# Performance work log

Hardware: AMD Instinct MI355X
Metric: run time of the kernel (lower is better)

## Reference

```python
import jax, jax.numpy as jnp
import numpy as np
from jax import lax

# Resolved Optuna hyperparameters
NPOINTS = (512, 256, 128)
RADII = (0.2, 0.4, 0.8)
KS = (32, 32, 32)
BN_EPS = 1e-5


def _fps_single(pts, npoint):
    """Farthest point sampling on one cloud. pts: (N,3) -> (npoint,) int32."""
    N = pts.shape[0]
    def step(carry, _):
        dists, last = carry
        d = jnp.sum((pts - pts[last]) ** 2, axis=-1)
        dists = jnp.minimum(dists, d)
        nxt = jnp.argmax(dists).astype(jnp.int32)
        return (dists, nxt), last
    init = (jnp.full((N,), 1e10, pts.dtype), jnp.int32(0))
    (_, _), idx = lax.scan(step, init, None, length=npoint)
    return idx


def _set_abstraction(xyz, feat, W, b, radius, k, npoint):
    """xyz: (B,N,3), feat: (B,N,C_in) -> new_xyz (B,S,3), new_feat (B,S,C_out)."""
    B, N, _ = xyz.shape
    fps_idx = jax.vmap(lambda p: _fps_single(p, npoint))(xyz)          # (B,S)
    new_xyz = jax.vmap(lambda x, i: x[i])(xyz, fps_idx)                # (B,S,3)
    # ball query: squared distances centers -> all points
    d2 = jnp.sum((new_xyz[:, :, None, :] - xyz[:, None, :, :]) ** 2, axis=-1)  # (B,S,N)
    valid = d2 <= radius * radius
    ar = jnp.arange(N, dtype=jnp.int32)
    gi = jnp.where(valid, ar[None, None, :], N)                        # invalid -> N
    gi = jnp.sort(gi, axis=-1)[:, :, :k]                               # first k in index order
    first = gi[:, :, :1]
    gi = jnp.where(gi == N, first, gi)                                 # pad with first valid (center itself)
    g_xyz = jax.vmap(lambda x, i: x[i])(xyz, gi)                       # (B,S,k,3)
    rel = g_xyz - new_xyz[:, :, None, :]
    g_feat = jax.vmap(lambda x, i: x[i])(feat, gi)                     # (B,S,k,C_in)
    h = jnp.concatenate([rel, g_feat], axis=-1)                        # (B,S,k,3+C_in)
    h = jax.nn.relu(jnp.einsum('bskc,co->bsko', h, W) + b)
    return new_xyz, jnp.max(h, axis=2)                                 # max-pool over group


def _bn(x, g, b):
    # nn.BatchNorm1d training-mode forward (batch statistics, biased var)
    m = x.mean(axis=0)
    v = x.var(axis=0)
    return (x - m) * lax.rsqrt(v + BN_EPS) * g + b


def setup_inputs() -> dict:
    key = jax.random.key(0)
    ks = jax.random.split(key, 8)
    def w(k, i, o):
        return (jax.random.normal(k, (i, o), jnp.float32) / np.sqrt(i)).astype(jnp.float32)
    return dict(
        points=jax.random.uniform(ks[0], (16, 4096, 3), jnp.float32),
        W1=w(ks[1], 3 + 3, 64),   b1=jnp.zeros((64,), jnp.float32),
        W2=w(ks[2], 64 + 3, 128), b2=jnp.zeros((128,), jnp.float32),
        W3=w(ks[3], 128 + 3, 256), b3=jnp.zeros((256,), jnp.float32),
        fc1_w=w(ks[4], 256, 256), fc1_b=jnp.zeros((256,), jnp.float32),
        fc2_w=w(ks[5], 256, 128), fc2_b=jnp.zeros((128,), jnp.float32),
        fc3_w=w(ks[6], 128, 12),  fc3_b=jnp.zeros((12,), jnp.float32),
        bn1_g=jnp.ones((256,), jnp.float32), bn1_b=jnp.zeros((256,), jnp.float32),
        bn2_g=jnp.ones((128,), jnp.float32), bn2_b=jnp.zeros((128,), jnp.float32),
    )


def reference(points, W1, b1, W2, b2, W3, b3, fc1_w, fc1_b, fc2_w, fc2_b,
              fc3_w, fc3_b, bn1_g, bn1_b, bn2_g, bn2_b):
    B = points.shape[0]
    xyz, feat = points, points
    for (W, bb, r, k, s) in ((W1, b1, RADII[0], KS[0], NPOINTS[0]),
                             (W2, b2, RADII[1], KS[1], NPOINTS[1]),
                             (W3, b3, RADII[2], KS[2], NPOINTS[2])):
        xyz, feat = _set_abstraction(xyz, feat, W, bb, r, k, s)
    f = jnp.max(feat, axis=1)                                          # (B, ch3)
    x = jax.nn.relu(_bn(f @ fc1_w + fc1_b, bn1_g, bn1_b))              # dropout: eval-mode identity
    x = jax.nn.relu(_bn(x @ fc2_w + fc2_b, bn2_g, bn2_b))
    x = x @ fc3_w + fc3_b
    return x.reshape(B, 4, 3)
```

## Files before the change

kernel.cpp:

```cpp
#include <hip/hip_runtime.h>
#include <hip/hip_bf16.h>


#define B_SZ 16

template<int CTRL>
__device__ __forceinline__ float dpp_mv(float v) {
    const int i = __float_as_int(v);
    const int r = __builtin_amdgcn_update_dpp(i, i, CTRL, 0xf, 0xf, false);
    return __int_as_float(r);
}

template<int N, int NPOINT, int BLOCK>
__global__ __launch_bounds__(BLOCK) void fps_kernel(
    const float* __restrict__ xyz,
    float* __restrict__ newxyz)
{
    constexpr int P  = N / BLOCK;
    constexpr int NW = BLOCK / 64;
    __shared__ float4 part[2][NW];

    const int b = blockIdx.x, tid = threadIdx.x;
    const int lane = tid & 63, w = tid >> 6;
    const float* xb = xyz + (size_t)b * N * 3;

    float px[P], py[P], pz[P], dd[P];
    const int base = tid * P;
#pragma unroll
    for (int i = 0; i < P; i++) {
        px[i] = xb[(base + i) * 3 + 0];
        py[i] = xb[(base + i) * 3 + 1];
        pz[i] = xb[(base + i) * 3 + 2];
        dd[i] = 1e10f;
    }
    float lx = xb[0], ly = xb[1], lz = xb[2];
    if (tid == 0) {
        float* o = newxyz + (size_t)b * NPOINT * 3;
        o[0] = lx; o[1] = ly; o[2] = lz;
    }

    for (int s = 1; s < NPOINT; s++) {
        float bv = -1.0f, bx = 0.0f, by = 0.0f, bz = 0.0f;
#pragma unroll
        for (int i = 0; i < P; i++) {
            const float dx = px[i] - lx, dy = py[i] - ly, dz = pz[i] - lz;
            const float d2 = __fadd_rn(__fadd_rn(__fmul_rn(dx, dx), __fmul_rn(dy, dy)),
                                       __fmul_rn(dz, dz));
            const float nd = fminf(dd[i], d2);
            dd[i] = nd;
            const bool gt = nd > bv;
            bv = gt ? nd : bv;
            bx = gt ? px[i] : bx;
            by = gt ? py[i] : by;
            bz = gt ? pz[i] : bz;
        }
        float v = bv;
        v = fmaxf(v, dpp_mv<0x111>(v));
        v = fmaxf(v, dpp_mv<0x112>(v));
        v = fmaxf(v, dpp_mv<0x114>(v));
        v = fmaxf(v, dpp_mv<0x118>(v));
        v = fmaxf(v, dpp_mv<0x142>(v));
        v = fmaxf(v, dpp_mv<0x143>(v));
        const float wmax = __uint_as_float(__builtin_amdgcn_readlane(__float_as_uint(v), 63));
        const unsigned long long mset = __ballot(bv == wmax);
        const int li = __ffsll(mset) - 1;
        const int buf = s & 1;
        if (lane == li) part[buf][w] = make_float4(bv, bx, by, bz);
        __syncthreads();
        float cv = -1.0f;
#pragma unroll
        for (int q = 0; q < NW; q++) {
            const float4 pq = part[buf][q];
            const bool gt = pq.x > cv;
            cv = gt ? pq.x : cv;
            lx = gt ? pq.y : lx;
            ly = gt ? pq.z : ly;
            lz = gt ? pq.w : lz;
        }
        if (tid == 0) {
            float* o = newxyz + ((size_t)b * NPOINT + s) * 3;
            o[0] = lx; o[1] = ly; o[2] = lz;
        }
    }
}

template<int N, int S, int CF, int COUT, int R>
__global__ __launch_bounds__(64) void sa_kernel(
    const float* __restrict__ xyz,
    const float* __restrict__ feat,
    const float* __restrict__ cent,
    const float* __restrict__ W,
    const float* __restrict__ bias,
    float* __restrict__ outf,
    const float r2)
{
    constexpr int K    = 32;
    constexpr int JT   = 16;
    constexpr int CIN  = CF + 3;
    constexpr int CINP = (CIN + 3) & ~3;
    constexpr int C4   = CIN & ~3;
    __shared__ int   gi[K];
    __shared__ float h[JT * CINP];

    const int s = blockIdx.x, b = blockIdx.y;
    const int lane = threadIdx.x;

    const float* xb = xyz  + (size_t)b * N * 3;
    const float* fb = feat + (size_t)b * N * CF;
    const float cx = cent[((size_t)b * S + s) * 3 + 0];
    const float cy = cent[((size_t)b * S + s) * 3 + 1];
    const float cz = cent[((size_t)b * S + s) * 3 + 2];

    constexpr int RND = N / 256;
    int total = 0, g0 = 0;
    for (int r0 = 0; r0 < RND; r0++) {
        if (total >= K) break;
        float xs[4], ys[4], zs[4];
#pragma unroll
        for (int c4 = 0; c4 < 4; c4++) {
            const int p = (r0 * 4 + c4) * 64 + lane;
            xs[c4] = xb[p * 3 + 0];
            ys[c4] = xb[p * 3 + 1];
            zs[c4] = xb[p * 3 + 2];
        }
#pragma unroll
        for (int c4 = 0; c4 < 4; c4++) {
            const int p = (r0 * 4 + c4) * 64 + lane;
            const float dx = xs[c4] - cx, dy = ys[c4] - cy, dz = zs[c4] - cz;
            const float d2 = __fadd_rn(__fadd_rn(__fmul_rn(dx, dx), __fmul_rn(dy, dy)),
                                       __fmul_rn(dz, dz));
            const bool v = (d2 <= r2);
            const unsigned long long bal = __ballot(v);
            if (total == 0 && bal != 0ull) g0 = (r0 * 4 + c4) * 64 + (__ffsll(bal) - 1);
            const int pos = total + __popcll(bal & ((1ull << lane) - 1ull));
            if (v && pos < K) gi[pos] = p;
            total += __popcll(bal);
        }
    }
    if (lane == 0 && total < K) {
        for (int q = total; q < K; q++) gi[q] = g0;
    }
    __syncthreads();

    float m[R];
#pragma unroll
    for (int r = 0; r < R; r++) m[r] = -1e30f;

    for (int pass = 0; pass < K / JT; pass++) {
        for (int jj = 0; jj < JT; jj++) {
            const int idx = gi[pass * JT + jj];
            for (int c = lane; c < CIN; c += 64) {
                float val;
                if (c < 3) {
                    const float cc = (c == 0) ? cx : ((c == 1) ? cy : cz);
                    val = xb[idx * 3 + c] - cc;
                } else {
                    val = fb[(size_t)idx * CF + (c - 3)];
                }
                h[jj * CINP + c] = val;
            }
        }
        __syncthreads();

        float acc[JT][R];
#pragma unroll
        for (int jj = 0; jj < JT; jj++)
#pragma unroll
            for (int r = 0; r < R; r++) acc[jj][r] = 0.0f;

        const float* wp = W + lane;
        int c = 0;
        for (; c < C4; c += 4) {
            float wv[4][R];
#pragma unroll
            for (int q = 0; q < 4; q++)
#pragma unroll
                for (int r = 0; r < R; r++)
                    wv[q][r] = wp[(size_t)(c + q) * COUT + r * 64];
#pragma unroll
            for (int jj = 0; jj < JT; jj++) {
                const float4 hv = *(const float4*)&h[jj * CINP + c];
#pragma unroll
                for (int r = 0; r < R; r++) {
                    acc[jj][r] = fmaf(hv.x, wv[0][r], acc[jj][r]);
                    acc[jj][r] = fmaf(hv.y, wv[1][r], acc[jj][r]);
                    acc[jj][r] = fmaf(hv.z, wv[2][r], acc[jj][r]);
                    acc[jj][r] = fmaf(hv.w, wv[3][r], acc[jj][r]);
                }
            }
        }
        for (; c < CIN; c++) {
            float wv[R];
#pragma unroll
            for (int r = 0; r < R; r++) wv[r] = wp[(size_t)c * COUT + r * 64];
#pragma unroll
            for (int jj = 0; jj < JT; jj++) {
                const float hv = h[jj * CINP + c];
#pragma unroll
                for (int r = 0; r < R; r++)
                    acc[jj][r] = fmaf(hv, wv[r], acc[jj][r]);
            }
        }
#pragma unroll
        for (int jj = 0; jj < JT; jj++)
#pragma unroll
            for (int r = 0; r < R; r++) m[r] = fmaxf(m[r], acc[jj][r]);
        __syncthreads();
    }

#pragma unroll
    for (int r = 0; r < R; r++) {
        const int o = r * 64 + lane;
        outf[((size_t)b * S + s) * COUT + o] = fmaxf(bias[o] + m[r], 0.0f);
    }
}

__global__ __launch_bounds__(256) void maxpool_kernel(
    const float* __restrict__ feat,
    float* __restrict__ out)
{
    const int b = blockIdx.x, o = threadIdx.x;
    const float* fb = feat + (size_t)b * 128 * 256 + o;
    float m = fb[0];
#pragma unroll 4
    for (int s1 = 1; s1 < 128; s1++) m = fmaxf(m, fb[(size_t)s1 * 256]);
    out[b * 256 + o] = m;
}

__global__ __launch_bounds__(256) void head_kernel(
    const float* __restrict__ f,
    const float* __restrict__ fc1_w, const float* __restrict__ fc1_b,
    const float* __restrict__ fc2_w, const float* __restrict__ fc2_b,
    const float* __restrict__ fc3_w, const float* __restrict__ fc3_b,
    const float* __restrict__ bn1_g, const float* __restrict__ bn1_b,
    const float* __restrict__ bn2_g, const float* __restrict__ bn2_b,
    float* __restrict__ out)
{
    __shared__ float fl[16 * 257];
    __shared__ float x1[16 * 257];
    __shared__ float x2[16 * 129];
    const int tid = threadIdx.x;

    for (int idx = tid; idx < 16 * 256; idx += 256) {
        const int r = idx >> 8, c = idx & 255;
        fl[r * 257 + c] = f[idx];
    }
    __syncthreads();

    {
        const int r = tid >> 4, g = tid & 15;
        float acc[16];
#pragma unroll
        for (int i = 0; i < 16; i++) acc[i] = fc1_b[g * 16 + i];
        const float* wrow = fc1_w + g * 16;
        for (int c = 0; c < 256; c++) {
            const float fv = fl[r * 257 + c];
            const float4* w4 = (const float4*)(wrow + (size_t)c * 256);
#pragma unroll
            for (int q = 0; q < 4; q++) {
                const float4 wv = w4[q];
                acc[q * 4 + 0] = fmaf(fv, wv.x, acc[q * 4 + 0]);
                acc[q * 4 + 1] = fmaf(fv, wv.y, acc[q * 4 + 1]);
                acc[q * 4 + 2] = fmaf(fv, wv.z, acc[q * 4 + 2]);
                acc[q * 4 + 3] = fmaf(fv, wv.w, acc[q * 4 + 3]);
            }
        }
#pragma unroll
        for (int i = 0; i < 16; i++) x1[r * 257 + g * 16 + i] = acc[i];
    }
    __syncthreads();
    {
        const int o = tid;
        float v[16];
#pragma unroll
        for (int r = 0; r < 16; r++) v[r] = x1[r * 257 + o];
        float m = 0.0f;
#pragma unroll
        for (int r = 0; r < 16; r++) m += v[r];
        m *= (1.0f / 16.0f);
        float var = 0.0f;
#pragma unroll
        for (int r = 0; r < 16; r++) { const float d = v[r] - m; var += d * d; }
        var *= (1.0f / 16.0f);
        const float sc = bn1_g[o] / sqrtf(var + 1e-5f);
        const float sh = bn1_b[o];
#pragma unroll
        for (int r = 0; r < 16; r++)
            x1[r * 257 + o] = fmaxf((v[r] - m) * sc + sh, 0.0f);
    }
    __syncthreads();
    {
        const int r = tid >> 4, g = tid & 15;
        float acc[8];
#pragma unroll
        for (int i = 0; i < 8; i++) acc[i] = fc2_b[g * 8 + i];
        const float* wrow = fc2_w + g * 8;
        for (int c = 0; c < 256; c++) {
            const float fv = x1[r * 257 + c];
            const float4* w4 = (const float4*)(wrow + (size_t)c * 128);
#pragma unroll
            for (int q = 0; q < 2; q++) {
                const float4 wv = w4[q];
                acc[q * 4 + 0] = fmaf(fv, wv.x, acc[q * 4 + 0]);
                acc[q * 4 + 1] = fmaf(fv, wv.y, acc[q * 4 + 1]);
                acc[q * 4 + 2] = fmaf(fv, wv.z, acc[q * 4 + 2]);
                acc[q * 4 + 3] = fmaf(fv, wv.w, acc[q * 4 + 3]);
            }
        }
#pragma unroll
        for (int i = 0; i < 8; i++) x2[r * 129 + g * 8 + i] = acc[i];
    }
    __syncthreads();
    if (tid < 128) {
        const int o = tid;
        float v[16];
#pragma unroll
        for (int r = 0; r < 16; r++) v[r] = x2[r * 129 + o];
        float m = 0.0f;
#pragma unroll
        for (int r = 0; r < 16; r++) m += v[r];
        m *= (1.0f / 16.0f);
        float var = 0.0f;
#pragma unroll
        for (int r = 0; r < 16; r++) { const float d = v[r] - m; var += d * d; }
        var *= (1.0f / 16.0f);
        const float sc = bn2_g[o] / sqrtf(var + 1e-5f);
        const float sh = bn2_b[o];
#pragma unroll
        for (int r = 0; r < 16; r++)
            x2[r * 129 + o] = fmaxf((v[r] - m) * sc + sh, 0.0f);
    }
    __syncthreads();
    if (tid < 192) {
        const int r = tid / 12, j = tid - r * 12;
        float acc = fc3_b[j];
        for (int c = 0; c < 128; c++)
            acc = fmaf(x2[r * 129 + c], fc3_w[c * 12 + j], acc);
        out[r * 12 + j] = acc;
    }
}

extern "C" void kernel_launch(void* const* d_in, const int* in_sizes, int n_in,
                              void* d_out, int out_size, void* d_ws, size_t ws_size,
                              hipStream_t stream) {
    const float* points = (const float*)d_in[0];
    const float* W1     = (const float*)d_in[1];
    const float* b1     = (const float*)d_in[2];
    const float* W2     = (const float*)d_in[3];
    const float* b2     = (const float*)d_in[4];
    const float* W3     = (const float*)d_in[5];
    const float* b3     = (const float*)d_in[6];
    const float* fc1_w  = (const float*)d_in[7];
    const float* fc1_b  = (const float*)d_in[8];
    const float* fc2_w  = (const float*)d_in[9];
    const float* fc2_b  = (const float*)d_in[10];
    const float* fc3_w  = (const float*)d_in[11];
    const float* fc3_b  = (const float*)d_in[12];
    const float* bn1_g  = (const float*)d_in[13];
    const float* bn1_b  = (const float*)d_in[14];
    const float* bn2_g  = (const float*)d_in[15];
    const float* bn2_b  = (const float*)d_in[16];
    float* out = (float*)d_out;

    float* ws   = (float*)d_ws;
    float* nx1  = ws;
    float* f1   = nx1 + 24576;
    float* nx2  = f1  + 524288;
    float* f2   = nx2 + 12288;
    float* nx3  = f2  + 524288;
    float* f3   = nx3 + 6144;
    float* fmx  = f3  + 524288;

    fps_kernel<4096, 512, 512><<<B_SZ, 512, 0, stream>>>(points, nx1);
    sa_kernel<4096, 512, 3, 64, 1><<<dim3(512, B_SZ), 64, 0, stream>>>(
        points, points, nx1, W1, b1, f1, (float)(0.2 * 0.2));
    fps_kernel<512, 256, 512><<<B_SZ, 512, 0, stream>>>(nx1, nx2);
    sa_kernel<512, 256, 64, 128, 2><<<dim3(256, B_SZ), 64, 0, stream>>>(
        nx1, f1, nx2, W2, b2, f2, (float)(0.4 * 0.4));
    fps_kernel<256, 128, 256><<<B_SZ, 256, 0, stream>>>(nx2, nx3);
    sa_kernel<256, 128, 128, 256, 4><<<dim3(128, B_SZ), 64, 0, stream>>>(
        nx2, f2, nx3, W3, b3, f3, (float)(0.8 * 0.8));
    maxpool_kernel<<<B_SZ, 256, 0, stream>>>(f3, fmx);
    head_kernel<<<1, 256, 0, stream>>>(fmx, fc1_w, fc1_b, fc2_w, fc2_b,
                                       fc3_w, fc3_b, bn1_g, bn1_b, bn2_g, bn2_b,
                                       out);
}
```

Before: 876.1 us.

## Use single-wave FPS for small clouds and tree-reduce per-thread argmax

The per-point argmax tracking in farthest point sampling becomes a tree max over the per-thread distance array, and the winning coordinates are recovered from a shared-memory copy of the cloud. Stages 2 and 3 (512 and 256 points) move to a new single-wave kernel that needs no __syncthreads, broadcasting the winner with readlane. Stage 1 drops from 512 to 256 threads, so each thread handles more points. The aim is to cut the per-step block synchronisation and serial select chain that dominate this latency-bound loop, at the cost of fewer threads doing more work each.

```diff
diff --git a/kernel.cpp b/kernel.cpp
--- a/kernel.cpp
+++ b/kernel.cpp
@@ -11,61 +11,82 @@
     return __int_as_float(r);
 }
 
+__device__ __forceinline__ float wave_max_f32(float x) {
+    float v = x;
+    v = fmaxf(v, dpp_mv<0x111>(v));
+    v = fmaxf(v, dpp_mv<0x112>(v));
+    v = fmaxf(v, dpp_mv<0x114>(v));
+    v = fmaxf(v, dpp_mv<0x118>(v));
+    v = fmaxf(v, dpp_mv<0x142>(v));
+    v = fmaxf(v, dpp_mv<0x143>(v));
+    return __uint_as_float(__builtin_amdgcn_readlane(__float_as_uint(v), 63));
+}
+
+__device__ __forceinline__ float read_lane_f32(float v, int l) {
+    return __uint_as_float(__builtin_amdgcn_readlane(__float_as_uint(v), l));
+}
+
 template<int N, int NPOINT, int BLOCK>
-__global__ __launch_bounds__(BLOCK) void fps_kernel(
+__global__ __launch_bounds__(BLOCK, 1) void fps_kernel(
     const float* __restrict__ xyz,
     float* __restrict__ newxyz)
 {
     constexpr int P  = N / BLOCK;
     constexpr int NW = BLOCK / 64;
+    __shared__ float pts[N * 3];
     __shared__ float4 part[2][NW];
 
     const int b = blockIdx.x, tid = threadIdx.x;
     const int lane = tid & 63, w = tid >> 6;
     const float* xb = xyz + (size_t)b * N * 3;
 
+    for (int t = tid; t < N * 3; t += BLOCK) pts[t] = xb[t];
+    __syncthreads();
+
     float px[P], py[P], pz[P], dd[P];
     const int base = tid * P;
 #pragma unroll
     for (int i = 0; i < P; i++) {
-        px[i] = xb[(base + i) * 3 + 0];
-        py[i] = xb[(base + i) * 3 + 1];
-        pz[i] = xb[(base + i) * 3 + 2];
+        px[i] = pts[(base + i) * 3 + 0];
+        py[i] = pts[(base + i) * 3 + 1];
+        pz[i] = pts[(base + i) * 3 + 2];
         dd[i] = 1e10f;
     }
-    float lx = xb[0], ly = xb[1], lz = xb[2];
+    float lx = pts[0], ly = pts[1], lz = pts[2];
     if (tid == 0) {
         float* o = newxyz + (size_t)b * NPOINT * 3;
         o[0] = lx; o[1] = ly; o[2] = lz;
     }
 
     for (int s = 1; s < NPOINT; s++) {
-        float bv = -1.0f, bx = 0.0f, by = 0.0f, bz = 0.0f;
 #pragma unroll
         for (int i = 0; i < P; i++) {
             const float dx = px[i] - lx, dy = py[i] - ly, dz = pz[i] - lz;
             const float d2 = __fadd_rn(__fadd_rn(__fmul_rn(dx, dx), __fmul_rn(dy, dy)),
                                        __fmul_rn(dz, dz));
-            const float nd = fminf(dd[i], d2);
-            dd[i] = nd;
-            const bool gt = nd > bv;
-            bv = gt ? nd : bv;
-            bx = gt ? px[i] : bx;
-            by = gt ? py[i] : by;
-            bz = gt ? pz[i] : bz;
-        }
-        float v = bv;
-        v = fmaxf(v, dpp_mv<0x111>(v));
-        v = fmaxf(v, dpp_mv<0x112>(v));
-        v = fmaxf(v, dpp_mv<0x114>(v));
-        v = fmaxf(v, dpp_mv<0x118>(v));
-        v = fmaxf(v, dpp_mv<0x142>(v));
-        v = fmaxf(v, dpp_mv<0x143>(v));
-        const float wmax = __uint_as_float(__builtin_amdgcn_readlane(__float_as_uint(v), 63));
-        const unsigned long long mset = __ballot(bv == wmax);
+            dd[i] = fminf(dd[i], d2);
+        }
+        float red[P];
+#pragma unroll
+        for (int i = 0; i < P; i++) red[i] = dd[i];
+#pragma unroll
+        for (int st = P / 2; st > 0; st >>= 1)
+#pragma unroll
+            for (int i = 0; i < P; i++)
+                if (i < st) red[i] = fmaxf(red[i], red[i + st]);
+        const float tm = red[0];
+
+        const float wmax = wave_max_f32(tm);
+        const unsigned long long mset = __ballot(tm == wmax);
         const int li = __ffsll(mset) - 1;
         const int buf = s & 1;
-        if (lane == li) part[buf][w] = make_float4(bv, bx, by, bz);
+        if (lane == li) {
+            unsigned mm = 0u;
+#pragma unroll
+            for (int i = 0; i < P; i++) mm |= (dd[i] == tm) ? (1u << i) : 0u;
+            const int g = base + (__ffs(mm) - 1);
+            part[buf][w] = make_float4(tm, pts[g * 3 + 0], pts[g * 3 + 1], pts[g * 3 + 2]);
+        }
         __syncthreads();
         float cv = -1.0f;
 #pragma unroll
@@ -78,6 +99,74 @@
             lz = gt ? pq.w : lz;
         }
         if (tid == 0) {
+            float* o = newxyz + ((size_t)b * NPOINT + s) * 3;
+            o[0] = lx; o[1] = ly; o[2] = lz;
+        }
+    }
+}
+
+template<int N, int NPOINT>
+__global__ __launch_bounds__(64, 1) void fps_wave_kernel(
+    const float* __restrict__ xyz,
+    float* __restrict__ newxyz)
+{
+    constexpr int P = N / 64;
+    __shared__ float pts[N * 3];
+
+    const int b = blockIdx.x, lane = threadIdx.x;
+    const float* xb = xyz + (size_t)b * N * 3;
+
+    for (int t = lane; t < N * 3; t += 64) pts[t] = xb[t];
+    __syncthreads();
+
+    float px[P], py[P], pz[P], dd[P];
+    const int base = lane * P;
+#pragma unroll
+    for (int i = 0; i < P; i++) {
+        px[i] = pts[(base + i) * 3 + 0];
+        py[i] = pts[(base + i) * 3 + 1];
+        pz[i] = pts[(base + i) * 3 + 2];
+        dd[i] = 1e10f;
+    }
+    float lx = pts[0], ly = pts[1], lz = pts[2];
+    if (lane == 0) {
+        float* o = newxyz + (size_t)b * NPOINT * 3;
+        o[0] = lx; o[1] = ly; o[2] = lz;
+    }
+
+    for (int s = 1; s < NPOINT; s++) {
+#pragma unroll
+        for (int i = 0; i < P; i++) {
+            const float dx = px[i] - lx, dy = py[i] - ly, dz = pz[i] - lz;
+            const float d2 = __fadd_rn(__fadd_rn(__fmul_rn(dx, dx), __fmul_rn(dy, dy)),
+                                       __fmul_rn(dz, dz));
+            dd[i] = fminf(dd[i], d2);
+        }
+        float red[P];
+#pragma unroll
+        for (int i = 0; i < P; i++) red[i] = dd[i];
+#pragma unroll
+        for (int st = P / 2; st > 0; st >>= 1)
+#pragma unroll
+            for (int i = 0; i < P; i++)
+                if (i < st) red[i] = fmaxf(red[i], red[i + st]);
+        const float tm = red[0];
+
+        const float wmax = wave_max_f32(tm);
+        const unsigned long long mset = __ballot(tm == wmax);
+        const int li = __ffsll(mset) - 1;
+        float wx = 0.0f, wy = 0.0f, wz = 0.0f;
+        if (lane == li) {
+            unsigned mm = 0u;
+#pragma unroll
+            for (int i = 0; i < P; i++) mm |= (dd[i] == tm) ? (1u << i) : 0u;
+            const int g = base + (__ffs(mm) - 1);
+            wx = pts[g * 3 + 0]; wy = pts[g * 3 + 1]; wz = pts[g * 3 + 2];
+        }
+        lx = read_lane_f32(wx, li);
+        ly = read_lane_f32(wy, li);
+        lz = read_lane_f32(wz, li);
+        if (lane == 0) {
             float* o = newxyz + ((size_t)b * NPOINT + s) * 3;
             o[0] = lx; o[1] = ly; o[2] = lz;
         }
@@ -371,13 +460,13 @@
     float* f3   = nx3 + 6144;
     float* fmx  = f3  + 524288;
 
-    fps_kernel<4096, 512, 512><<<B_SZ, 512, 0, stream>>>(points, nx1);
+    fps_kernel<4096, 512, 256><<<B_SZ, 256, 0, stream>>>(points, nx1);
     sa_kernel<4096, 512, 3, 64, 1><<<dim3(512, B_SZ), 64, 0, stream>>>(
         points, points, nx1, W1, b1, f1, (float)(0.2 * 0.2));
-    fps_kernel<512, 256, 512><<<B_SZ, 512, 0, stream>>>(nx1, nx2);
+    fps_wave_kernel<512, 256><<<B_SZ, 64, 0, stream>>>(nx1, nx2);
     sa_kernel<512, 256, 64, 128, 2><<<dim3(256, B_SZ), 64, 0, stream>>>(
         nx1, f1, nx2, W2, b2, f2, (float)(0.4 * 0.4));
-    fps_kernel<256, 128, 256><<<B_SZ, 256, 0, stream>>>(nx2, nx3);
+    fps_wave_kernel<256, 128><<<B_SZ, 64, 0, stream>>>(nx2, nx3);
     sa_kernel<256, 128, 128, 256, 4><<<dim3(128, B_SZ), 64, 0, stream>>>(
         nx2, f2, nx3, W3, b3, f3, (float)(0.8 * 0.8));
     maxpool_kernel<<<B_SZ, 256, 0, stream>>>(f3, fmx);
```

Measured after the change: 973.6 us. 11.1% more time.
